# Optimization experiments

Measured on AMD Instinct MI355X. Metric: run time of the kernel, lower is better.

Reference implementation:

```python
import jax, jax.numpy as jnp
import numpy as np

D = 1024      # hidden_size
H = 16        # num_attention_heads
HD = D // H   # head_dim
FF = 4096     # intermediate_size
EPS = 1e-5

def layernorm(x, g, b):
    mu = jnp.mean(x, axis=-1, keepdims=True)
    var = jnp.mean(jnp.square(x - mu), axis=-1, keepdims=True)
    return (x - mu) * jax.lax.rsqrt(var + EPS) * g + b

def setup_inputs() -> dict:
    key = jax.random.key(0)
    ks = jax.random.split(key, 16)
    s = 0.02
    return {
        "x":   jax.random.normal(ks[0], (4, 1024, D), jnp.float32),
        "wq":  jax.random.normal(ks[1], (D, D), jnp.float32) * s,
        "bq":  jnp.zeros((D,), jnp.float32),
        "wk":  jax.random.normal(ks[2], (D, D), jnp.float32) * s,
        "bk":  jnp.zeros((D,), jnp.float32),
        "wv":  jax.random.normal(ks[3], (D, D), jnp.float32) * s,
        "bv":  jnp.zeros((D,), jnp.float32),
        "wo":  jax.random.normal(ks[4], (D, D), jnp.float32) * s,
        "bo":  jnp.zeros((D,), jnp.float32),
        "w1":  jax.random.normal(ks[5], (D, FF), jnp.float32) * s,
        "b1":  jnp.zeros((FF,), jnp.float32),
        "w2":  jax.random.normal(ks[6], (FF, D), jnp.float32) * s,
        "b2":  jnp.zeros((D,), jnp.float32),
        "ln1_g": jnp.ones((D,), jnp.float32),
        "ln1_b": jnp.zeros((D,), jnp.float32),
        "ln2_g": jnp.ones((D,), jnp.float32),
        "ln2_b": jnp.zeros((D,), jnp.float32),
    }

def reference(x, wq, bq, wk, bk, wv, bv, wo, bo, w1, b1, w2, b2,
              ln1_g, ln1_b, ln2_g, ln2_b):
    B, S, _ = x.shape
    # --- pre-LN multi-head attention (per-head linears fused as one GEMM) ---
    h = layernorm(x, ln1_g, ln1_b)
    q = (h @ wq + bq).reshape(B, S, H, HD).transpose(0, 2, 1, 3)  # [B,H,S,hd]
    k = (h @ wk + bk).reshape(B, S, H, HD).transpose(0, 2, 1, 3)
    v = (h @ wv + bv).reshape(B, S, H, HD).transpose(0, 2, 1, 3)
    scores = jnp.einsum('bhqd,bhkd->bhqk', q, k) / np.sqrt(HD).astype(x.dtype)
    weights = jax.nn.softmax(scores, axis=-1)  # dropout p=0 -> identity
    attn = jnp.einsum('bhqk,bhkd->bhqd', weights, v)
    attn = attn.transpose(0, 2, 1, 3).reshape(B, S, D)
    x = x + attn @ wo + bo
    # --- pre-LN feed-forward with exact GELU ---
    h2 = layernorm(x, ln2_g, ln2_b)
    ffn = jax.nn.gelu(h2 @ w1 + b1, approximate=False) @ w2 + b2
    return x + ffn
```

## Files before the change

kernel.cpp:

```cpp
#include <hip/hip_runtime.h>
#include <hip/hip_bf16.h>
#include <cstdint>

#define S_LEN  1024
#define DMODEL 1024
#define NTOK   4096
#define NHEAD  16
#define HDIM   64
#define FFDIM  4096
#define NBATCH 4
#define QSCALE 0.1803368801f

using bf16x8 = __attribute__((ext_vector_type(8))) short;
using f32x4  = __attribute__((ext_vector_type(4))) float;

__device__ __forceinline__ ushort f2bf(float f) {
  union { float f; uint32_t u; } a; a.f = f;
  uint32_t u = a.u;
  u += 0x7FFFu + ((u >> 16) & 1u);
  return (ushort)(u >> 16);
}
__device__ __forceinline__ ushort f2bf_hw(float f) {
  uint32_t r;
  asm("v_cvt_pk_bf16_f32 %0, %1, %1" : "=v"(r) : "v"(f));
  return (ushort)r;
}
__device__ __forceinline__ float bf2f(ushort u) {
  union { uint32_t u; float f; } c; c.u = ((uint32_t)u) << 16; return c.f;
}
__device__ __forceinline__ void st_out(float* C, long i, float v) { C[i] = v; }
__device__ __forceinline__ void st_out(ushort* C, long i, float v) { C[i] = f2bf(v); }

__device__ __forceinline__ void gld_lds16(const void* g, void* l) {
  __builtin_amdgcn_global_load_lds((const __attribute__((address_space(1))) void*)g,
                                   (__attribute__((address_space(3))) void*)l, 16, 0, 0);
}

__global__ __launch_bounds__(256) void ln_kernel(const float* __restrict__ x,
    const float* __restrict__ g, const float* __restrict__ b,
    ushort* __restrict__ out) {
  int row = blockIdx.x;
  int tid = threadIdx.x;
  const float4* xr = (const float4*)(x + (long)row * DMODEL);
  float4 v = xr[tid];
  float s  = v.x + v.y + v.z + v.w;
  float s2 = v.x*v.x + v.y*v.y + v.z*v.z + v.w*v.w;
  for (int off = 32; off; off >>= 1) { s += __shfl_down(s, off); s2 += __shfl_down(s2, off); }
  __shared__ float red[8];
  int wid = tid >> 6, lane = tid & 63;
  if (lane == 0) { red[wid] = s; red[wid + 4] = s2; }
  __syncthreads();
  if (tid == 0) {
    red[0] = red[0] + red[1] + red[2] + red[3];
    red[4] = red[4] + red[5] + red[6] + red[7];
  }
  __syncthreads();
  float mu  = red[0] * (1.0f / DMODEL);
  float var = red[4] * (1.0f / DMODEL) - mu * mu;
  float rs  = rsqrtf(var + 1e-5f);
  float4 gg = ((const float4*)g)[tid];
  float4 bb = ((const float4*)b)[tid];
  ushort4 o;
  o.x = f2bf((v.x - mu) * rs * gg.x + bb.x);
  o.y = f2bf((v.y - mu) * rs * gg.y + bb.y);
  o.z = f2bf((v.z - mu) * rs * gg.z + bb.z);
  o.w = f2bf((v.w - mu) * rs * gg.w + bb.w);
  ((ushort4*)(out + (long)row * DMODEL))[tid] = o;
}

__global__ __launch_bounds__(256) void concat3(const float* __restrict__ a,
    const float* __restrict__ b, const float* __restrict__ c, float* __restrict__ o) {
  int i = blockIdx.x * 256 + threadIdx.x;
  o[i] = (i < 1024) ? a[i] : ((i < 2048) ? b[i - 1024] : c[i - 2048]);
}

template <int NP>
__global__ __launch_bounds__(256) void reduce_add(
    const ushort* __restrict__ parts, const float* __restrict__ bias,
    float* __restrict__ out) {
  long i = (long)blockIdx.x * 256 + threadIdx.x;
  const long PSTRIDE = (long)NTOK * DMODEL / 4;
  float4 acc = ((const float4*)out)[i];
  float4 b = ((const float4*)bias)[i & 255];
  acc.x += b.x; acc.y += b.y; acc.z += b.z; acc.w += b.w;
#pragma unroll
  for (int z = 0; z < NP; ++z) {
    ushort4 u = ((const ushort4*)parts)[z * PSTRIDE + i];
    acc.x += bf2f(u.x); acc.y += bf2f(u.y); acc.z += bf2f(u.z); acc.w += bf2f(u.w);
  }
  ((float4*)out)[i] = acc;
}

template <int NP>
__global__ __launch_bounds__(256) void reduce_ln(
    const ushort* __restrict__ parts, const float* __restrict__ xres,
    const float* __restrict__ bias, float* __restrict__ out,
    const float* __restrict__ g, const float* __restrict__ bln,
    ushort* __restrict__ hout) {
  int row = blockIdx.x, tid = threadIdx.x;
  long i = (long)row * 256 + tid;
  const long PSTRIDE = (long)NTOK * DMODEL / 4;
  float4 v = ((const float4*)xres)[i];
  float4 b = ((const float4*)bias)[tid];
  v.x += b.x; v.y += b.y; v.z += b.z; v.w += b.w;
#pragma unroll
  for (int z = 0; z < NP; ++z) {
    ushort4 u = ((const ushort4*)parts)[z * PSTRIDE + i];
    v.x += bf2f(u.x); v.y += bf2f(u.y); v.z += bf2f(u.z); v.w += bf2f(u.w);
  }
  ((float4*)out)[i] = v;
  float s  = v.x + v.y + v.z + v.w;
  float s2 = v.x*v.x + v.y*v.y + v.z*v.z + v.w*v.w;
  for (int off = 32; off; off >>= 1) { s += __shfl_down(s, off); s2 += __shfl_down(s2, off); }
  __shared__ float red[8];
  int wid = tid >> 6, lane = tid & 63;
  if (lane == 0) { red[wid] = s; red[wid + 4] = s2; }
  __syncthreads();
  if (tid == 0) {
    red[0] = red[0] + red[1] + red[2] + red[3];
    red[4] = red[4] + red[5] + red[6] + red[7];
  }
  __syncthreads();
  float mu  = red[0] * (1.0f / DMODEL);
  float var = red[4] * (1.0f / DMODEL) - mu * mu;
  float rs  = rsqrtf(var + 1e-5f);
  float4 gg = ((const float4*)g)[tid];
  float4 bb = ((const float4*)bln)[tid];
  ushort4 o;
  o.x = f2bf((v.x - mu) * rs * gg.x + bb.x);
  o.y = f2bf((v.y - mu) * rs * gg.y + bb.y);
  o.z = f2bf((v.z - mu) * rs * gg.z + bb.z);
  o.w = f2bf((v.w - mu) * rs * gg.w + bb.w);
  ((ushort4*)hout)[i] = o;
}

template <typename TIN>
__global__ __launch_bounds__(256) void transpose_cvt(const TIN* __restrict__ in,
    ushort* __restrict__ out, int ldin, int ldout,
    long inZhi, long inZlo, long outZ) {
  int z = blockIdx.z;
  in  += (long)(z >> 4) * inZhi + (long)(z & 15) * inZlo;
  out += (long)z * outZ;
  __shared__ float tile[32][33];
  int c0 = blockIdx.x * 32, r0 = blockIdx.y * 32;
  int tx = threadIdx.x, ty = threadIdx.y;
  for (int i = ty; i < 32; i += 8)
    tile[i][tx] = bf2f(in[(long)(r0 + i) * ldin + c0 + tx]);
  __syncthreads();
  for (int i = ty; i < 32; i += 8)
    out[(long)(c0 + i) * ldout + r0 + tx] = f2bf(tile[tx][i]);
}

__global__ __launch_bounds__(256) void wt4(const float* __restrict__ wq,
    const float* __restrict__ wk, const float* __restrict__ wv,
    const float* __restrict__ wo, ushort* __restrict__ outb) {
  int z = blockIdx.z;
  const float* in = (z == 0) ? wq : (z == 1) ? wk : (z == 2) ? wv : wo;
  ushort* out = outb + (long)z * DMODEL * DMODEL;
  __shared__ float tile[32][33];
  int c0 = blockIdx.x * 32, r0 = blockIdx.y * 32;
  int tx = threadIdx.x, ty = threadIdx.y;
  for (int i = ty; i < 32; i += 8)
    tile[i][tx] = in[(long)(r0 + i) * DMODEL + c0 + tx];
  __syncthreads();
  for (int i = ty; i < 32; i += 8)
    out[(long)(c0 + i) * DMODEL + r0 + tx] = f2bf(tile[tx][i]);
}

__global__ __launch_bounds__(256) void w12t(const float* __restrict__ w1,
    const float* __restrict__ w2, ushort* __restrict__ w1T, ushort* __restrict__ w2T) {
  int z = blockIdx.z;
  __shared__ float tile[32][33];
  int tx = threadIdx.x, ty = threadIdx.y;
  if (z == 0) {
    int c0 = blockIdx.x * 32, r0 = blockIdx.y * 32;
    for (int i = ty; i < 32; i += 8)
      tile[i][tx] = w1[(long)(r0 + i) * FFDIM + c0 + tx];
    __syncthreads();
    for (int i = ty; i < 32; i += 8)
      w1T[(long)(c0 + i) * DMODEL + r0 + tx] = f2bf(tile[tx][i]);
  } else {
    int c0 = blockIdx.y * 32, r0 = blockIdx.x * 32;
    for (int i = ty; i < 32; i += 8)
      tile[i][tx] = w2[(long)(r0 + i) * DMODEL + c0 + tx];
    __syncthreads();
    for (int i = ty; i < 32; i += 8)
      w2T[(long)(c0 + i) * FFDIM + r0 + tx] = f2bf(tile[tx][i]);
  }
}

template <int ACT, bool BIAS, typename TOUT>
__global__ __launch_bounds__(256) void gemm_bt(
    const ushort* __restrict__ A, const ushort* __restrict__ BT, TOUT* __restrict__ C,
    const float* __restrict__ bias,
    int M, int K, int lda, int ldb, int ldc,
    long aZlo, long bZlo, long cZlo) {
  __shared__ __align__(16) ushort lA[2][128 * 64];
  __shared__ __align__(16) ushort lB[2][128 * 64];
  int z = blockIdx.z;
  A  += (long)z * aZlo;
  BT += (long)z * bZlo;
  C  += (long)z * cZlo;
  int gx = gridDim.x;
  int nwg = gx * gridDim.y;
  int lin = blockIdx.x + gx * blockIdx.y;
  int wg = (lin & 7) * (nwg >> 3) + (lin >> 3);
  int n0 = (wg / gx) * 128, m0 = (wg % gx) * 128;
  int tid = threadIdx.x, lane = tid & 63, wid = tid >> 6;
  int wr = wid >> 1, wc = wid & 1;
  int lrow = lane >> 3;
  int swz = ((lane & 7) ^ lrow) << 3;
  f32x4 acc[4][4];
#pragma unroll
  for (int i = 0; i < 4; i++)
#pragma unroll
    for (int j = 0; j < 4; j++) acc[i][j] = (f32x4){0.f, 0.f, 0.f, 0.f};

  long lda8 = (long)8 * lda, ldb8 = (long)8 * ldb;
  const ushort* aBase = A + (long)(n0 + wid * 32 + lrow) * lda + swz;
  const ushort* bBase = BT + (long)(m0 + wid * 32 + lrow) * ldb + swz;
  auto STAGE = [&](int kt, int buf) {
    int ko = kt << 6;
#pragma unroll
    for (int c = 0; c < 4; ++c) {
      int ch = (wid << 2) | c;
      gld_lds16(aBase + c * lda8 + ko, &lA[buf][ch << 9]);
      gld_lds16(bBase + c * ldb8 + ko, &lB[buf][ch << 9]);
    }
  };
  int kOff0 = (((lane >> 4) ^ (lane & 7)) << 3);
  int kOff1 = (((4 | (lane >> 4)) ^ (lane & 7)) << 3);

  int nK = K >> 6;
  STAGE(0, 0);
  for (int kt = 0; kt < nK; ++kt) {
    int cur = kt & 1;
    if (kt + 1 < nK) {
      STAGE(kt + 1, cur ^ 1);
      asm volatile("s_waitcnt vmcnt(8)" ::: "memory");
    } else {
      asm volatile("s_waitcnt vmcnt(0)" ::: "memory");
    }
    __builtin_amdgcn_s_barrier();
    __builtin_amdgcn_sched_barrier(0);
    const ushort* baseA = &lA[cur][((wr << 6) + (lane & 15)) * 64];
    const ushort* baseB = &lB[cur][((wc << 6) + (lane & 15)) * 64];
#pragma unroll
    for (int kk = 0; kk < 2; ++kk) {
      int kfs = kk ? kOff1 : kOff0;
      bf16x8 af[4], bfr[4];
#pragma unroll
      for (int i = 0; i < 4; i++) {
        af[i]  = *(const bf16x8*)(baseA + i * 1024 + kfs);
        bfr[i] = *(const bf16x8*)(baseB + i * 1024 + kfs);
      }
#pragma unroll
      for (int i = 0; i < 4; i++)
#pragma unroll
        for (int j = 0; j < 4; j++)
          acc[i][j] = __builtin_amdgcn_mfma_f32_16x16x32_bf16(af[i], bfr[j], acc[i][j], 0, 0, 0);
    }
    asm volatile("s_waitcnt lgkmcnt(0)" ::: "memory");
    __builtin_amdgcn_s_barrier();
    __builtin_amdgcn_sched_barrier(0);
  }
#pragma unroll
  for (int i = 0; i < 4; i++) {
    int rbase = n0 + wr * 64 + i * 16 + ((lane >> 4) << 2);
#pragma unroll
    for (int j = 0; j < 4; j++) {
      int col = m0 + wc * 64 + j * 16 + (lane & 15);
      float bv = BIAS ? bias[col] : 0.0f;
#pragma unroll
      for (int q = 0; q < 4; q++) {
        float vv = acc[i][j][q] + bv;
        if (ACT == 1) vv = 0.5f * vv * (1.0f + erff(vv * 0.70710678118f));
        if (ACT == 2 && col < DMODEL) vv *= QSCALE;
        st_out(C, (long)(rbase + q) * ldc + col, vv);
      }
    }
  }
}

template <int ACT, bool BIAS, typename TOUT>
__global__ __launch_bounds__(512, 2) void gemm256(
    const ushort* __restrict__ A, const ushort* __restrict__ BT, TOUT* __restrict__ C,
    const float* __restrict__ bias,
    int K, int lda, int ldb, int ldc, long aZlo, long bZlo, long cZlo) {
  __shared__ __align__(16) ushort lA[2][256 * 64];
  __shared__ __align__(16) ushort lB[2][256 * 64];
  int z = blockIdx.z;
  A  += (long)z * aZlo;
  BT += (long)z * bZlo;
  C  += (long)z * cZlo;
  int gx = gridDim.x;
  int nwg = gx * gridDim.y;
  int lin = blockIdx.x + gx * blockIdx.y;
  int wg = (lin & 7) * (nwg >> 3) + (lin >> 3);
  int n0 = (wg / gx) * 256, m0 = (wg % gx) * 256;
  int tid = threadIdx.x, lane = tid & 63, wid = tid >> 6;
  int wm = wid >> 2, wn = wid & 3;
  int lo = lane & 15, hi = lane >> 4;
  int l7 = lane & 7;
  int srow = tid >> 3;
  int skg  = (tid & 7) ^ (srow & 7);
  const ushort* gA = A + (long)(n0 + srow) * lda + (skg << 3);
  const ushort* gB = BT + (long)(m0 + srow) * ldb + (skg << 3);
  long lda64 = (long)64 * lda, ldb64 = (long)64 * ldb;

  f32x4 acc[8][4];
#pragma unroll
  for (int i = 0; i < 8; ++i)
#pragma unroll
    for (int j = 0; j < 4; ++j) acc[i][j] = (f32x4){0.f, 0.f, 0.f, 0.f};

  auto STG = [&](int kt, int buf, int c) {
    if (c < 4)
      gld_lds16(gA + c * lda64 + (kt << 6), &lA[buf][c * 4096 + wid * 512]);
    else
      gld_lds16(gB + (c - 4) * ldb64 + (kt << 6), &lB[buf][(c - 4) * 4096 + wid * 512]);
  };
  int kOff0 = ((hi ^ l7) << 3);
  int kOff1 = (((4 | hi) ^ l7) << 3);

  int nK = K >> 6;
  STG(0, 0, 4); STG(0, 0, 5); STG(0, 0, 6); STG(0, 0, 7);
  STG(0, 0, 0); STG(0, 0, 1); STG(0, 0, 2); STG(0, 0, 3);
  STG(1, 1, 4); STG(1, 1, 5); STG(1, 1, 6); STG(1, 1, 7);
  asm volatile("s_waitcnt vmcnt(4)" ::: "memory");
  __builtin_amdgcn_s_barrier();

  for (int t = 0; t < nK; ++t) {
    int cur = t & 1, nxt = cur ^ 1;
    const ushort* baseA = &lA[cur][(wm * 128 + lo) * 64];
    const ushort* baseB = &lB[cur][(wn * 64 + lo) * 64];
    bf16x8 bfr[4][2];
#pragma unroll
    for (int p = 0; p < 4; ++p) {
      if (p == 0) {
#pragma unroll
        for (int j = 0; j < 4; ++j) {
          bfr[j][0] = *(const bf16x8*)(baseB + j * 1024 + kOff0);
          bfr[j][1] = *(const bf16x8*)(baseB + j * 1024 + kOff1);
        }
      }
      bf16x8 afr[2][2];
#pragma unroll
      for (int ii = 0; ii < 2; ++ii) {
        afr[ii][0] = *(const bf16x8*)(baseA + (p * 2 + ii) * 1024 + kOff0);
        afr[ii][1] = *(const bf16x8*)(baseA + (p * 2 + ii) * 1024 + kOff1);
      }
      if (p == 0 && t + 1 < nK) { STG(t + 1, nxt, 0); STG(t + 1, nxt, 1); }
      if (p == 1 && t + 1 < nK) { STG(t + 1, nxt, 2); STG(t + 1, nxt, 3); }
      if (p == 2 && t + 2 < nK) { STG(t + 2, cur, 4); STG(t + 2, cur, 5); }
      if (p == 3 && t + 2 < nK) { STG(t + 2, cur, 6); STG(t + 2, cur, 7); }
      __builtin_amdgcn_s_barrier();
      asm volatile("s_waitcnt lgkmcnt(0)" ::: "memory");
      __builtin_amdgcn_sched_barrier(0);
      __builtin_amdgcn_s_setprio(1);
#pragma unroll
      for (int ii = 0; ii < 2; ++ii)
#pragma unroll
        for (int j = 0; j < 4; ++j)
#pragma unroll
          for (int kk = 0; kk < 2; ++kk)
            acc[p * 2 + ii][j] = __builtin_amdgcn_mfma_f32_16x16x32_bf16(
                afr[ii][kk], bfr[j][kk], acc[p * 2 + ii][j], 0, 0, 0);
      __builtin_amdgcn_s_setprio(0);
      __builtin_amdgcn_sched_barrier(0);
      if (p == 3 && t + 1 < nK) {
        if (t + 2 < nK) asm volatile("s_waitcnt vmcnt(4)" ::: "memory");
        else            asm volatile("s_waitcnt vmcnt(0)" ::: "memory");
      }
      __builtin_amdgcn_s_barrier();
    }
  }

#pragma unroll
  for (int i = 0; i < 8; ++i) {
    int rbase = n0 + wm * 128 + i * 16 + hi * 4;
#pragma unroll
    for (int j = 0; j < 4; ++j) {
      int colg = m0 + wn * 64 + j * 16 + lo;
      float bv = BIAS ? bias[colg] : 0.0f;
#pragma unroll
      for (int q = 0; q < 4; ++q) {
        float vv = acc[i][j][q] + bv;
        if (ACT == 1) vv = 0.5f * vv * (1.0f + erff(vv * 0.70710678118f));
        if (ACT == 2 && colg < DMODEL) vv *= QSCALE;
        long idx = (long)(rbase + q) * ldc + colg;
        st_out(C, idx, vv);
      }
    }
  }
}

#define QBLK 64
#define KBLK 128
__global__ __launch_bounds__(256) void flash_attn(
    const ushort* __restrict__ qkv, const ushort* __restrict__ vt,
    ushort* __restrict__ attn) {
  __shared__ __align__(16) ushort lK[2][KBLK * 64];
  __shared__ __align__(16) ushort lV[2][64 * KBLK];
  __shared__ __align__(16) ushort lP[4 * 16 * KBLK];

  int qt = blockIdx.x, bh = blockIdx.z;
  int b = bh >> 4, hh = bh & 15;
  int tid = threadIdx.x, lane = tid & 63, wid = tid >> 6;
  int lo = lane & 15, hi = lane >> 4;
  int lrow = lane >> 3;
  int swz8 = ((lane & 7) ^ lrow) << 3;

  const ushort* Qg = qkv + (long)(b * 1024 + qt * QBLK) * 3072 + hh * 64;
  const ushort* Kg = qkv + (long)(b * 1024) * 3072 + 1024 + hh * 64;
  const ushort* Vg = vt + (long)bh * 64 * 1024;
  ushort* lPw = lP + wid * (16 * KBLK);

  bf16x8 kOnes;
#pragma unroll
  for (int i = 0; i < 8; ++i) kOnes[i] = (short)0x3F80;

  auto STAGE = [&](int t, int buf) {
#pragma unroll
    for (int c = 0; c < 4; ++c) {
      int ch = (wid << 2) | c;
      int rb = (ch << 3) + lrow;
      gld_lds16(Kg + (long)(t * KBLK + rb) * 3072 + swz8, &lK[buf][ch << 9]);
    }
#pragma unroll
    for (int c = 0; c < 4; ++c) {
      int ch = (wid << 2) | c;
      int hd = (ch << 2) + hi;
      gld_lds16(Vg + (long)hd * 1024 + t * KBLK + ((lo ^ (hd & 7)) << 3), &lV[buf][ch << 9]);
    }
  };

#pragma unroll
  for (int c = 0; c < 2; ++c) {
    int ch = wid * 2 + c;
    int rb = ch * 8 + lrow;
    gld_lds16(Qg + (long)rb * 3072 + swz8, &lP[ch << 9]);
  }
  STAGE(0, 0);
  asm volatile("s_waitcnt vmcnt(8)" ::: "memory");
  __builtin_amdgcn_sched_barrier(0);
  bf16x8 a_q[2];
#pragma unroll
  for (int kk = 0; kk < 2; ++kk)
    a_q[kk] = *(const bf16x8*)&lP[(wid * 16 + lo) * 64 + (((kk * 4 + hi) ^ (lo & 7)) << 3)];
  asm volatile("s_waitcnt lgkmcnt(0)" ::: "memory");
  __builtin_amdgcn_sched_barrier(0);
  __builtin_amdgcn_s_barrier();

  float m_run[4];
#pragma unroll
  for (int q = 0; q < 4; ++q) m_run[q] = -1e30f;
  f32x4 acc_o[4];
#pragma unroll
  for (int j = 0; j < 4; ++j) acc_o[j] = (f32x4){0.f, 0.f, 0.f, 0.f};
  f32x4 acc_l = (f32x4){0.f, 0.f, 0.f, 0.f};

  for (int t = 0; t < 8; ++t) {
    int cur = t & 1;
    if (t + 1 < 8) {
      STAGE(t + 1, cur ^ 1);
      asm volatile("s_waitcnt vmcnt(8)" ::: "memory");
    } else {
      asm volatile("s_waitcnt vmcnt(0)" ::: "memory");
    }
    __builtin_amdgcn_s_barrier();
    __builtin_amdgcn_sched_barrier(0);

    f32x4 s[8];
#pragma unroll
    for (int j = 0; j < 8; ++j) s[j] = (f32x4){0.f, 0.f, 0.f, 0.f};
    __builtin_amdgcn_s_setprio(1);
#pragma unroll
    for (int kk = 0; kk < 2; ++kk) {
      int slot = ((kk * 4 + hi) ^ (lo & 7)) << 3;
#pragma unroll
      for (int j = 0; j < 8; ++j) {
        bf16x8 bk = *(const bf16x8*)&lK[cur][(j * 16 + lo) * 64 + slot];
        s[j] = __builtin_amdgcn_mfma_f32_16x16x32_bf16(a_q[kk], bk, s[j], 0, 0, 0);
      }
    }
    __builtin_amdgcn_s_setprio(0);

    float alpha[4];
#pragma unroll
    for (int q = 0; q < 4; ++q) {
      float m = fmaxf(fmaxf(fmaxf(s[0][q], s[1][q]), fmaxf(s[2][q], s[3][q])),
                      fmaxf(fmaxf(s[4][q], s[5][q]), fmaxf(s[6][q], s[7][q])));
#pragma unroll
      for (int off = 1; off < 16; off <<= 1) m = fmaxf(m, __shfl_xor(m, off));
      float mnew = fmaxf(m_run[q], m);
      alpha[q] = __builtin_amdgcn_exp2f(m_run[q] - mnew);
      m_run[q] = mnew;
    }
#pragma unroll
    for (int j = 0; j < 8; ++j)
#pragma unroll
      for (int q = 0; q < 4; ++q) {
        float e = __builtin_amdgcn_exp2f(s[j][q] - m_run[q]);
        int row = hi * 4 + q;
        int col = j * 16 + lo;
        lPw[row * KBLK + (col ^ ((row & 7) << 3))] = f2bf_hw(e);
      }

#pragma unroll
    for (int q = 0; q < 4; ++q) acc_l[q] *= alpha[q];
#pragma unroll
    for (int j = 0; j < 4; ++j)
#pragma unroll
      for (int q = 0; q < 4; ++q) acc_o[j][q] *= alpha[q];
    __builtin_amdgcn_s_setprio(1);
#pragma unroll
    for (int ks = 0; ks < 4; ++ks) {
      int slot = ((ks * 4 + hi) ^ (lo & 7)) << 3;
      bf16x8 ap = *(const bf16x8*)&lPw[lo * KBLK + slot];
      acc_l = __builtin_amdgcn_mfma_f32_16x16x32_bf16(ap, kOnes, acc_l, 0, 0, 0);
#pragma unroll
      for (int j = 0; j < 4; ++j) {
        bf16x8 bv = *(const bf16x8*)&lV[cur][(j * 16 + lo) * KBLK + slot];
        acc_o[j] = __builtin_amdgcn_mfma_f32_16x16x32_bf16(ap, bv, acc_o[j], 0, 0, 0);
      }
    }
    __builtin_amdgcn_s_setprio(0);
    asm volatile("s_waitcnt lgkmcnt(0)" ::: "memory");
    __builtin_amdgcn_s_barrier();
    __builtin_amdgcn_sched_barrier(0);
  }

#pragma unroll
  for (int q = 0; q < 4; ++q) {
    float linv = 1.0f / acc_l[q];
    int qrow = qt * QBLK + wid * 16 + hi * 4 + q;
#pragma unroll
    for (int j = 0; j < 4; ++j)
      attn[(long)(b * 1024 + qrow) * 1024 + hh * 64 + j * 16 + lo] = f2bf(acc_o[j][q] * linv);
  }
}

extern "C" void kernel_launch(void* const* d_in, const int* in_sizes, int n_in,
                              void* d_out, int out_size, void* d_ws, size_t ws_size,
                              hipStream_t stream) {
  const float* x    = (const float*)d_in[0];
  const float* wq   = (const float*)d_in[1];
  const float* bq   = (const float*)d_in[2];
  const float* wk   = (const float*)d_in[3];
  const float* bk   = (const float*)d_in[4];
  const float* wv   = (const float*)d_in[5];
  const float* bv   = (const float*)d_in[6];
  const float* wo   = (const float*)d_in[7];
  const float* bo   = (const float*)d_in[8];
  const float* w1   = (const float*)d_in[9];
  const float* b1   = (const float*)d_in[10];
  const float* w2   = (const float*)d_in[11];
  const float* b2   = (const float*)d_in[12];
  const float* ln1g = (const float*)d_in[13];
  const float* ln1b = (const float*)d_in[14];
  const float* ln2g = (const float*)d_in[15];
  const float* ln2b = (const float*)d_in[16];
  float* out = (float*)d_out;

  char* ws = (char*)d_ws;
  size_t off = 0;
  auto alloc = [&](size_t bytes) { void* p = ws + off; off += (bytes + 255) & ~(size_t)255; return p; };
  ushort* h     = (ushort*)alloc((size_t)NTOK * DMODEL * 2);
  ushort* wqkvT = (ushort*)alloc((size_t)3 * DMODEL * DMODEL * 2);
  ushort* woT   = (ushort*)alloc((size_t)DMODEL * DMODEL * 2);
  float*  bqkv  = (float*)alloc((size_t)3 * DMODEL * 4);
  ushort* qkv   = (ushort*)alloc((size_t)NTOK * 3 * DMODEL * 2);
  ushort* vt    = (ushort*)alloc((size_t)64 * HDIM * S_LEN * 2);
  ushort* attn  = (ushort*)alloc((size_t)NTOK * DMODEL * 2);
  ushort* w1T   = (ushort*)alloc((size_t)DMODEL * FFDIM * 2);
  ushort* w2T   = (ushort*)alloc((size_t)FFDIM * DMODEL * 2);
  ushort* gact  = (ushort*)alloc((size_t)NTOK * FFDIM * 2);
  ushort* woPart  = qkv;
  ushort* ffnPart = qkv;

  dim3 tb32(32, 8);
  hipLaunchKernelGGL(wt4, dim3(DMODEL/32, DMODEL/32, 4), tb32, 0, stream,
                     wq, wk, wv, wo, wqkvT);
  hipLaunchKernelGGL(w12t, dim3(FFDIM/32, DMODEL/32, 2), tb32, 0, stream,
                     w1, w2, w1T, w2T);
  hipLaunchKernelGGL(concat3, dim3(12), dim3(256), 0, stream, bq, bk, bv, bqkv);

  hipLaunchKernelGGL(ln_kernel, dim3(NTOK), dim3(256), 0, stream, x, ln1g, ln1b, h);

  hipLaunchKernelGGL((gemm_bt<2, true, ushort>), dim3(24, 32, 1), dim3(256), 0, stream,
                     h, wqkvT, qkv, bqkv,
                     3 * DMODEL, DMODEL, DMODEL, DMODEL, 3 * DMODEL, 0L, 0L, 0L);

  hipLaunchKernelGGL((transpose_cvt<ushort>), dim3(HDIM/32, S_LEN/32, 64), tb32, 0, stream,
                     qkv + 2 * DMODEL, vt, 3 * DMODEL, S_LEN,
                     (long)S_LEN * 3 * DMODEL, 64L, (long)HDIM * S_LEN);

  hipLaunchKernelGGL(flash_attn, dim3(16, 1, 64), dim3(256), 0, stream, qkv, vt, attn);

  hipLaunchKernelGGL((gemm_bt<0, false, ushort>), dim3(8, 32, 2), dim3(256), 0, stream,
                     attn, woT, woPart, (const float*)nullptr,
                     DMODEL, 512, DMODEL, DMODEL, DMODEL,
                     512L, 512L, (long)NTOK * DMODEL);
  hipLaunchKernelGGL((reduce_ln<2>), dim3(4096), dim3(256), 0, stream,
                     woPart, x, bo, out, ln2g, ln2b, h);
  hipLaunchKernelGGL((gemm256<1, true, ushort>), dim3(16, 16, 1), dim3(512), 0, stream,
                     h, w1T, gact, b1, DMODEL, DMODEL, DMODEL, FFDIM, 0L, 0L, 0L);
  hipLaunchKernelGGL((gemm256<0, false, ushort>), dim3(4, 16, 4), dim3(512), 0, stream,
                     gact, w2T, ffnPart, (const float*)nullptr,
                     1024, FFDIM, FFDIM, DMODEL, 1024L, 1024L, (long)NTOK * DMODEL);
  hipLaunchKernelGGL((reduce_add<4>), dim3(4096), dim3(256), 0, stream,
                     ffnPart, b2, out);
  (void)in_sizes; (void)n_in; (void)out_size; (void)ws_size;
}
```

Baseline: 249.0 us.

## Switch 256x256 GEMM to 32x32x16 MFMA tiles and use it for QKV projection

Rewrites the big-tile GEMM's inner loop to use 32x32x16 bf16 MFMA instructions with 4x2 accumulator fragments per wave instead of 16x16x32 with 8x4 fragments. This cuts the number of LDS fragment reads and MFMA issues per k-step. The QKV projection also moves from the smaller 128-tile gemm_bt kernel to this 256-tile kernel, with a 12x16 grid of 512-thread blocks. The larger tiles mean fewer workgroups for the QKV GEMM (192), and the epilogue uses a different row mapping that must match the 32x32 MFMA output layout.

Result: no change. 245.9 us (-1.2%).

```diff
diff --git a/kernel.cpp b/kernel.cpp
--- a/kernel.cpp
+++ b/kernel.cpp
@@ -13,6 +13,7 @@
 
 using bf16x8 = __attribute__((ext_vector_type(8))) short;
 using f32x4  = __attribute__((ext_vector_type(4))) float;
+using f32x16 = __attribute__((ext_vector_type(16))) float;
 
 __device__ __forceinline__ ushort f2bf(float f) {
   union { float f; uint32_t u; } a; a.f = f;
@@ -283,7 +284,7 @@
 }
 
 template <int ACT, bool BIAS, typename TOUT>
-__global__ __launch_bounds__(512, 2) void gemm256(
+__global__ __launch_bounds__(512, 2) void gemm32(
     const ushort* __restrict__ A, const ushort* __restrict__ BT, TOUT* __restrict__ C,
     const float* __restrict__ bias,
     int K, int lda, int ldb, int ldc, long aZlo, long bZlo, long cZlo) {
@@ -300,19 +301,20 @@
   int n0 = (wg / gx) * 256, m0 = (wg % gx) * 256;
   int tid = threadIdx.x, lane = tid & 63, wid = tid >> 6;
   int wm = wid >> 2, wn = wid & 3;
-  int lo = lane & 15, hi = lane >> 4;
-  int l7 = lane & 7;
+  int l31 = lane & 31, lhi = lane >> 5, l7 = lane & 7;
   int srow = tid >> 3;
   int skg  = (tid & 7) ^ (srow & 7);
   const ushort* gA = A + (long)(n0 + srow) * lda + (skg << 3);
   const ushort* gB = BT + (long)(m0 + srow) * ldb + (skg << 3);
   long lda64 = (long)64 * lda, ldb64 = (long)64 * ldb;
 
-  f32x4 acc[8][4];
-#pragma unroll
-  for (int i = 0; i < 8; ++i)
-#pragma unroll
-    for (int j = 0; j < 4; ++j) acc[i][j] = (f32x4){0.f, 0.f, 0.f, 0.f};
+  f32x16 acc[4][2];
+#pragma unroll
+  for (int i = 0; i < 4; ++i)
+#pragma unroll
+    for (int j = 0; j < 2; ++j)
+#pragma unroll
+      for (int q = 0; q < 16; ++q) acc[i][j][q] = 0.f;
 
   auto STG = [&](int kt, int buf, int c) {
     if (c < 4)
@@ -320,8 +322,6 @@
     else
       gld_lds16(gB + (c - 4) * ldb64 + (kt << 6), &lB[buf][(c - 4) * 4096 + wid * 512]);
   };
-  int kOff0 = ((hi ^ l7) << 3);
-  int kOff1 = (((4 | hi) ^ l7) << 3);
 
   int nK = K >> 6;
   STG(0, 0, 4); STG(0, 0, 5); STG(0, 0, 6); STG(0, 0, 7);
@@ -332,24 +332,24 @@
 
   for (int t = 0; t < nK; ++t) {
     int cur = t & 1, nxt = cur ^ 1;
-    const ushort* baseA = &lA[cur][(wm * 128 + lo) * 64];
-    const ushort* baseB = &lB[cur][(wn * 64 + lo) * 64];
-    bf16x8 bfr[4][2];
+    const ushort* baseA = &lA[cur][(wm * 128 + l31) * 64];
+    const ushort* baseB = &lB[cur][(wn * 64 + l31) * 64];
+    bf16x8 bfr[2][4];
 #pragma unroll
     for (int p = 0; p < 4; ++p) {
+      int gslot = (((2 * p + lhi) ^ l7) << 3);
       if (p == 0) {
 #pragma unroll
-        for (int j = 0; j < 4; ++j) {
-          bfr[j][0] = *(const bf16x8*)(baseB + j * 1024 + kOff0);
-          bfr[j][1] = *(const bf16x8*)(baseB + j * 1024 + kOff1);
-        }
-      }
-      bf16x8 afr[2][2];
-#pragma unroll
-      for (int ii = 0; ii < 2; ++ii) {
-        afr[ii][0] = *(const bf16x8*)(baseA + (p * 2 + ii) * 1024 + kOff0);
-        afr[ii][1] = *(const bf16x8*)(baseA + (p * 2 + ii) * 1024 + kOff1);
-      }
+        for (int cf = 0; cf < 2; ++cf)
+#pragma unroll
+          for (int ks = 0; ks < 4; ++ks)
+            bfr[cf][ks] = *(const bf16x8*)(baseB + cf * 32 * 64 +
+                                           (((2 * ks + lhi) ^ l7) << 3));
+      }
+      bf16x8 afr[4];
+#pragma unroll
+      for (int rf = 0; rf < 4; ++rf)
+        afr[rf] = *(const bf16x8*)(baseA + rf * 32 * 64 + gslot);
       if (p == 0 && t + 1 < nK) { STG(t + 1, nxt, 0); STG(t + 1, nxt, 1); }
       if (p == 1 && t + 1 < nK) { STG(t + 1, nxt, 2); STG(t + 1, nxt, 3); }
       if (p == 2 && t + 2 < nK) { STG(t + 2, cur, 4); STG(t + 2, cur, 5); }
@@ -359,13 +359,11 @@
       __builtin_amdgcn_sched_barrier(0);
       __builtin_amdgcn_s_setprio(1);
 #pragma unroll
-      for (int ii = 0; ii < 2; ++ii)
-#pragma unroll
-        for (int j = 0; j < 4; ++j)
-#pragma unroll
-          for (int kk = 0; kk < 2; ++kk)
-            acc[p * 2 + ii][j] = __builtin_amdgcn_mfma_f32_16x16x32_bf16(
-                afr[ii][kk], bfr[j][kk], acc[p * 2 + ii][j], 0, 0, 0);
+      for (int rf = 0; rf < 4; ++rf)
+#pragma unroll
+        for (int cf = 0; cf < 2; ++cf)
+          acc[rf][cf] = __builtin_amdgcn_mfma_f32_32x32x16_bf16(
+              afr[rf], bfr[cf][p], acc[rf][cf], 0, 0, 0);
       __builtin_amdgcn_s_setprio(0);
       __builtin_amdgcn_sched_barrier(0);
       if (p == 3 && t + 1 < nK) {
@@ -377,19 +375,18 @@
   }
 
 #pragma unroll
-  for (int i = 0; i < 8; ++i) {
-    int rbase = n0 + wm * 128 + i * 16 + hi * 4;
-#pragma unroll
-    for (int j = 0; j < 4; ++j) {
-      int colg = m0 + wn * 64 + j * 16 + lo;
+  for (int rf = 0; rf < 4; ++rf) {
+#pragma unroll
+    for (int cf = 0; cf < 2; ++cf) {
+      int colg = m0 + wn * 64 + cf * 32 + l31;
       float bv = BIAS ? bias[colg] : 0.0f;
 #pragma unroll
-      for (int q = 0; q < 4; ++q) {
-        float vv = acc[i][j][q] + bv;
+      for (int r = 0; r < 16; ++r) {
+        int rowg = n0 + wm * 128 + rf * 32 + (r & 3) + 8 * (r >> 2) + 4 * lhi;
+        float vv = acc[rf][cf][r] + bv;
         if (ACT == 1) vv = 0.5f * vv * (1.0f + erff(vv * 0.70710678118f));
         if (ACT == 2 && colg < DMODEL) vv *= QSCALE;
-        long idx = (long)(rbase + q) * ldc + colg;
-        st_out(C, idx, vv);
+        st_out(C, (long)rowg * ldc + colg, vv);
       }
     }
   }
@@ -588,9 +585,8 @@
 
   hipLaunchKernelGGL(ln_kernel, dim3(NTOK), dim3(256), 0, stream, x, ln1g, ln1b, h);
 
-  hipLaunchKernelGGL((gemm_bt<2, true, ushort>), dim3(24, 32, 1), dim3(256), 0, stream,
-                     h, wqkvT, qkv, bqkv,
-                     3 * DMODEL, DMODEL, DMODEL, DMODEL, 3 * DMODEL, 0L, 0L, 0L);
+  hipLaunchKernelGGL((gemm32<2, true, ushort>), dim3(12, 16, 1), dim3(512), 0, stream,
+                     h, wqkvT, qkv, bqkv, DMODEL, DMODEL, DMODEL, 3 * DMODEL, 0L, 0L, 0L);
 
   hipLaunchKernelGGL((transpose_cvt<ushort>), dim3(HDIM/32, S_LEN/32, 64), tb32, 0, stream,
                      qkv + 2 * DMODEL, vt, 3 * DMODEL, S_LEN,
@@ -604,9 +600,9 @@
                      512L, 512L, (long)NTOK * DMODEL);
   hipLaunchKernelGGL((reduce_ln<2>), dim3(4096), dim3(256), 0, stream,
                      woPart, x, bo, out, ln2g, ln2b, h);
-  hipLaunchKernelGGL((gemm256<1, true, ushort>), dim3(16, 16, 1), dim3(512), 0, stream,
+  hipLaunchKernelGGL((gemm32<1, true, ushort>), dim3(16, 16, 1), dim3(512), 0, stream,
                      h, w1T, gact, b1, DMODEL, DMODEL, DMODEL, FFDIM, 0L, 0L, 0L);
-  hipLaunchKernelGGL((gemm256<0, false, ushort>), dim3(4, 16, 4), dim3(512), 0, stream,
+  hipLaunchKernelGGL((gemm32<0, false, ushort>), dim3(4, 16, 4), dim3(512), 0, stream,
                      gact, w2T, ffnPart, (const float*)nullptr,
                      1024, FFDIM, FFDIM, DMODEL, 1024L, 1024L, (long)NTOK * DMODEL);
   hipLaunchKernelGGL((reduce_add<4>), dim3(4096), dim3(256), 0, stream,
```
